# Kernel optimization log

Hardware: AMD Instinct MI355X
Metric: run time of the kernel (lower is better)

Reference implementation:

```python
import jax, jax.numpy as jnp
import numpy as np

N, HID, K = 256, 64, 2
B, T_ENC, T_DEC = 64, 12, 12
IN_DIM, OUT_DIM = 2, 1
NUM_SUPPORTS = 2
M = NUM_SUPPORTS * K + 1  # identity + K hops per support


def setup_inputs() -> dict:
    key = jax.random.key(0)
    ks = jax.random.split(key, 16)

    def w(k, shape, scale=0.05):
        return jax.random.normal(k, shape, dtype=jnp.float32) * scale

    def support(k):
        S = jax.random.uniform(k, (N, N), dtype=jnp.float32)
        return S / jnp.sum(S, axis=1, keepdims=True)  # random-walk normalized

    F0e = IN_DIM + HID   # encoder layer-0 concat(input, hidden) feature dim
    F1 = HID + HID       # layer-1 feature dim
    F0d = OUT_DIM + HID  # decoder layer-0 feature dim
    return {
        "encoder_inputs": jax.random.normal(ks[0], (B, T_ENC, N, IN_DIM), dtype=jnp.float32),
        "decoder_inputs": jax.random.normal(ks[1], (B, T_DEC, N, OUT_DIM), dtype=jnp.float32),
        "support0": support(ks[2]),
        "support1": support(ks[3]),
        "enc0_Wg": w(ks[4], (F0e, M, 2 * HID)), "enc0_bg": jnp.ones((2 * HID,), jnp.float32),
        "enc0_Wc": w(ks[5], (F0e, M, HID)),     "enc0_bc": jnp.zeros((HID,), jnp.float32),
        "enc1_Wg": w(ks[6], (F1, M, 2 * HID)),  "enc1_bg": jnp.ones((2 * HID,), jnp.float32),
        "enc1_Wc": w(ks[7], (F1, M, HID)),      "enc1_bc": jnp.zeros((HID,), jnp.float32),
        "dec0_Wg": w(ks[8], (F0d, M, 2 * HID)), "dec0_bg": jnp.ones((2 * HID,), jnp.float32),
        "dec0_Wc": w(ks[9], (F0d, M, HID)),     "dec0_bc": jnp.zeros((HID,), jnp.float32),
        "dec1_Wg": w(ks[10], (F1, M, 2 * HID)), "dec1_bg": jnp.ones((2 * HID,), jnp.float32),
        "dec1_Wc": w(ks[11], (F1, M, HID)),     "dec1_bc": jnp.zeros((HID,), jnp.float32),
        "proj_W": w(ks[12], (HID, OUT_DIM), 0.1),
        "proj_b": jnp.zeros((OUT_DIM,), jnp.float32),
    }


def _diff_conv(supports, x, h, W, b, in_dim):
    # x: (B, N*in_dim), h: (B, N*HID), W: (F, M, O) matching torch flatten order (f*M+m)
    Bsz = x.shape[0]
    xs = jnp.concatenate([x.reshape(Bsz, N, in_dim), h.reshape(Bsz, N, HID)], axis=-1)
    mats = [xs]
    for S in supports:
        x0 = xs
        x1 = jnp.einsum('mn,bnf->bmf', S, xs)
        mats.append(x1)
        for _ in range(2, K + 1):
            x2 = 2.0 * jnp.einsum('mn,bnf->bmf', S, x1) - x0  # Chebyshev recurrence
            mats.append(x2)
            x1, x0 = x2, x1
    X = jnp.stack(mats, axis=2)  # (B, N, M, F)
    out = jnp.einsum('bnmf,fmo->bno', X, W) + b
    return out.reshape(Bsz, -1)


def _cell(supports, x, h, Wg, bg, Wc, bc, in_dim):
    # DCGRUCell: sigmoid gates from diffusion conv, tanh candidate, GRU update
    Bsz = x.shape[0]
    ru = jax.nn.sigmoid(_diff_conv(supports, x, h, Wg, bg, in_dim)).reshape(Bsz, N, 2 * HID)
    r = ru[..., :HID].reshape(Bsz, N * HID)
    u = ru[..., HID:].reshape(Bsz, N * HID)
    c = jnp.tanh(_diff_conv(supports, x, r * h, Wc, bc, in_dim))
    return u * h + (1.0 - u) * c


def _forward(encoder_inputs, decoder_inputs, support0, support1,
             enc0_Wg, enc0_bg, enc0_Wc, enc0_bc, enc1_Wg, enc1_bg, enc1_Wc, enc1_bc,
             dec0_Wg, dec0_bg, dec0_Wc, dec0_bc, dec1_Wg, dec1_bg, dec1_Wc, dec1_bc,
             proj_W, proj_b):
    sup = (support0, support1)
    Bsz = encoder_inputs.shape[0]
    # encoder: (B,T,N,D) -> (T,B,N*D); zero initial hidden
    cur = jnp.transpose(encoder_inputs, (1, 0, 2, 3)).reshape(T_ENC, Bsz, N * IN_DIM)
    enc_params = [(enc0_Wg, enc0_bg, enc0_Wc, enc0_bc, IN_DIM),
                  (enc1_Wg, enc1_bg, enc1_Wc, enc1_bc, HID)]
    h_enc = []
    for (Wg, bg, Wc, bc, ind) in enc_params:
        h0 = jnp.zeros((Bsz, N * HID), cur.dtype)
        def estep(h, x, Wg=Wg, bg=bg, Wc=Wc, bc=bc, ind=ind):
            hn = _cell(sup, x, h, Wg, bg, Wc, bc, ind)
            return hn, hn
        hT, cur = jax.lax.scan(estep, h0, cur)
        h_enc.append(hT)
    # decoder (eval mode: no teacher forcing, dropout off); go symbol = zeros
    dec_params = [(dec0_Wg, dec0_bg, dec0_Wc, dec0_bc, OUT_DIM),
                  (dec1_Wg, dec1_bg, dec1_Wc, dec1_bc, HID)]
    go = jnp.zeros((Bsz, N * OUT_DIM), cur.dtype)

    def dstep(carry, _):
        hs, cur_in = carry
        out = cur_in
        new_hs = []
        for i, (Wg, bg, Wc, bc, ind) in enumerate(dec_params):
            hn = _cell(sup, out, hs[i], Wg, bg, Wc, bc, ind)
            out = hn
            new_hs.append(hn)
        proj = (jnp.einsum('bnh,ho->bno', out.reshape(Bsz, N, HID), proj_W) + proj_b)
        proj = proj.reshape(Bsz, N * OUT_DIM)
        return ((new_hs[0], new_hs[1]), proj), proj

    _, outs = jax.lax.scan(dstep, ((h_enc[0], h_enc[1]), go), None, length=T_DEC)
    outs = outs.reshape(T_DEC, Bsz, N, OUT_DIM)
    return jnp.transpose(outs, (1, 0, 2, 3))  # (B, T_DEC, N, OUT_DIM)


def reference(encoder_inputs, decoder_inputs, support0, support1,
              enc0_Wg, enc0_bg, enc0_Wc, enc0_bc, enc1_Wg, enc1_bg, enc1_Wc, enc1_bc,
              dec0_Wg, dec0_bg, dec0_Wc, dec0_bc, dec1_Wg, dec1_bg, dec1_Wc, dec1_bc,
              proj_W, proj_b):
    return _forward(encoder_inputs, decoder_inputs, support0, support1,
                    enc0_Wg, enc0_bg, enc0_Wc, enc0_bc, enc1_Wg, enc1_bg, enc1_Wc, enc1_bc,
                    dec0_Wg, dec0_bg, dec0_Wc, dec0_bc, dec1_Wg, dec1_bg, dec1_Wc, dec1_bc,
                    proj_W, proj_b)
```

## Files before the change

kernel.cpp:

```cpp
#include <hip/hip_runtime.h>
#include <stdint.h>


typedef short short8 __attribute__((ext_vector_type(8)));
typedef float f32x4 __attribute__((ext_vector_type(4)));
typedef unsigned short ushort4v __attribute__((ext_vector_type(4)));
typedef unsigned long long u64;
typedef u64 u64x2 __attribute__((ext_vector_type(2)));

#define DEVI __device__ __forceinline__

DEVI unsigned short f2bf(float x) {
  unsigned int u = __builtin_bit_cast(unsigned int, x);
  u += 0x7FFFu + ((u >> 16) & 1u);
  return (unsigned short)(u >> 16);
}
DEVI u64 ald(const u64* p) { return __hip_atomic_load(p, __ATOMIC_RELAXED, __HIP_MEMORY_SCOPE_AGENT); }
DEVI void ast(u64* p, u64 v) { __hip_atomic_store(p, v, __ATOMIC_RELAXED, __HIP_MEMORY_SCOPE_AGENT); }
DEVI float aldf(const float* p) { return __hip_atomic_load(p, __ATOMIC_RELAXED, __HIP_MEMORY_SCOPE_AGENT); }
DEVI void astf(float* p, float v) { __hip_atomic_store(p, v, __ATOMIC_RELAXED, __HIP_MEMORY_SCOPE_AGENT); }

struct KP {
  const float* enc_in;
  const float* sup0; const float* sup1;
  const float* Wsrc[8];
  const float* bias[8];
  const float* prW; const float* prB;
  float* out;
  unsigned short* A;
  unsigned short* Wp[8];
  unsigned short* H0[2];
  unsigned short* H1[2];
  unsigned short* RH0;
  unsigned short* RH1;
  float* XD;
  unsigned* ctr;
};

__global__ void prep(KP p) {
  const int i = blockIdx.x, tid = threadIdx.x;
  {
    const int s = i & 1, r = i >> 1;
    const float* S = s ? p.sup1 : p.sup0;
    float acc = 0.f;
    for (int k = 0; k < 256; ++k) acc = fmaf(S[r * 256 + k], S[k * 256 + tid], acc);
    p.A[(2 * s + 0) * 65536 + r * 256 + tid] = f2bf(S[r * 256 + tid]);
    p.A[(2 * s + 1) * 65536 + r * 256 + tid] = f2bf(2.f * acc - (r == tid ? 1.f : 0.f));
  }
  {
    const int gtid = i * 256 + tid;
    const int Fs[8]  = {66, 66, 128, 128, 65, 65, 128, 128};
    const int Os[8]  = {128, 64, 128, 64, 128, 64, 128, 64};
    const int FPs[8] = {96, 96, 128, 128, 96, 96, 128, 128};
    for (int w = 0; w < 8; ++w) {
      const int FPw = FPs[w], KPw = 5 * FPw, tot = Os[w] * KPw;
      for (int e = gtid; e < tot; e += 512 * 256) {
        const int o = e / KPw, k2 = e - o * KPw, m = k2 / FPw, f = k2 - m * FPw;
        p.Wp[w][e] = f2bf((f < Fs[w]) ? p.Wsrc[w][(f * 5 + m) * Os[w] + o] : 0.f);
      }
    }
  }
  {
    const int gtid = i * 256 + tid;
    u64* z0 = (u64*)p.H0[0];
    u64* z1 = (u64*)p.H1[0];
    ast(z0 + 2 * gtid, 0); ast(z0 + 2 * gtid + 1, 0);
    ast(z1 + 2 * gtid, 0); ast(z1 + 2 * gtid + 1, 0);
  }
  if (i == 0 && tid < 64)
    __hip_atomic_store(p.ctr + tid * 64, 0u, __ATOMIC_RELAXED, __HIP_MEMORY_SCOPE_AGENT);
}

template<int IND, int FP, int MODE>
DEVI void dc_stage(int b, int n0, int tid,
                   const float* xf32,
                   const unsigned short* xbf,
                   const unsigned short* hrows,
                   const unsigned short* Amats,
                   const unsigned short* Wp, const float* bias,
                   f32x4 (&hreg)[2], f32x4 (&ureg)[2],
                   unsigned short* grows,
                   const float* projW, const float* projB,
                   float* outp, float* xdout,
                   unsigned short* xsT, unsigned short* Hbuf)
{
  constexpr int F = IND + 64;
  constexpr int O = (MODE == 0) ? 128 : 64;
  constexpr int KPW = 5 * FP;
  constexpr int XS = 264;
  constexpr int HS = 136;
  constexpr int NFT = FP / 16;
  constexpr int NOT_ = O / 16;
  constexpr int FT_W = (NFT + 3) / 4;
  constexpr int OT_W = (NOT_ + 3) / 4;

  const int wv8 = tid >> 6, ln = tid & 63;
  const int l15 = ln & 15, l4 = ln >> 4;
  const int wr = wv8 & 1, wc = wv8 >> 1;
  const int r0 = wr * 32;

  {
    u64 la[4], lb[4];
    const u64* src = (const u64*)hrows;
#pragma unroll
    for (int it = 0; it < 4; ++it) { const int g = tid + it * 512; la[it] = ald(src + 2 * g); lb[it] = ald(src + 2 * g + 1); }
#pragma unroll
    for (int it = 0; it < 4; ++it) {
      const int g = tid + it * 512, row = g >> 5, c = g & 31;
      u64x2 v; v[0] = la[it]; v[1] = lb[it];
      *reinterpret_cast<u64x2*>(&xsT[(IND + row) * XS + c * 8]) = v;
    }
  }
  if (IND == 64) {
    u64 la[4], lb[4];
    const u64* src = (const u64*)xbf;
#pragma unroll
    for (int it = 0; it < 4; ++it) { const int g = tid + it * 512; la[it] = ald(src + 2 * g); lb[it] = ald(src + 2 * g + 1); }
#pragma unroll
    for (int it = 0; it < 4; ++it) {
      const int g = tid + it * 512, row = g >> 5, c = g & 31;
      u64x2 v; v[0] = la[it]; v[1] = lb[it];
      *reinterpret_cast<u64x2*>(&xsT[row * XS + c * 8]) = v;
    }
  } else if (IND == 2) {
    const float v = xf32[tid];
    xsT[(tid & 1) * XS + (tid >> 1)] = f2bf(v);
  } else {
    if (tid < 256) xsT[tid] = xf32 ? f2bf(aldf(xf32 + tid)) : (unsigned short)0;
  }
  if (F < FP) {
    for (int e = tid; e < (FP - F) * 256; e += 512)
      xsT[(F + (e >> 8)) * XS + (e & 255)] = 0;
  }
  __syncthreads();
#pragma unroll
  for (int it = 0; it < FP / 8; ++it) {
    const int e = tid + it * 512, f = e >> 6, nl = e & 63;
    Hbuf[nl * HS + f] = xsT[f * XS + n0 + nl];
  }
  __syncthreads();

  f32x4 pacc[2][OT_W];
#pragma unroll
  for (int rt = 0; rt < 2; ++rt)
#pragma unroll
    for (int oi = 0; oi < OT_W; ++oi) pacc[rt][oi] = 0.f;

  auto proj_step = [&](int m) {
#pragma unroll
    for (int k0 = 0; k0 < FP; k0 += 32) {
      short8 af[2];
#pragma unroll
      for (int rt = 0; rt < 2; ++rt)
        af[rt] = *reinterpret_cast<const short8*>(&Hbuf[(r0 + rt * 16 + l15) * HS + k0 + l4 * 8]);
#pragma unroll
      for (int oi = 0; oi < OT_W; ++oi) {
        const int ot = wc + 4 * oi;
        if (ot < NOT_) {
          short8 bf = *reinterpret_cast<const short8*>(&Wp[(ot * 16 + l15) * KPW + m * FP + k0 + l4 * 8]);
#pragma unroll
          for (int rt = 0; rt < 2; ++rt)
            pacc[rt][oi] = __builtin_amdgcn_mfma_f32_16x16x32_bf16(af[rt], bf, pacc[rt][oi], 0, 0, 0);
        }
      }
    }
  };

  proj_step(0);

  for (int mi = 0; mi < 4; ++mi) {
    const unsigned short* Am = Amats + mi * 65536;
    f32x4 hacc[2][FT_W];
#pragma unroll
    for (int rt = 0; rt < 2; ++rt)
#pragma unroll
      for (int fi = 0; fi < FT_W; ++fi) hacc[rt][fi] = 0.f;

#pragma unroll
    for (int k0 = 0; k0 < 256; k0 += 32) {
      short8 af[2];
#pragma unroll
      for (int rt = 0; rt < 2; ++rt)
        af[rt] = *reinterpret_cast<const short8*>(&Am[(n0 + r0 + rt * 16 + l15) * 256 + k0 + l4 * 8]);
#pragma unroll
      for (int fi = 0; fi < FT_W; ++fi) {
        const int ft = wc + 4 * fi;
        if (ft < NFT) {
          short8 bf = *reinterpret_cast<const short8*>(&xsT[(ft * 16 + l15) * XS + k0 + l4 * 8]);
#pragma unroll
          for (int rt = 0; rt < 2; ++rt)
            hacc[rt][fi] = __builtin_amdgcn_mfma_f32_16x16x32_bf16(af[rt], bf, hacc[rt][fi], 0, 0, 0);
        }
      }
    }
    __syncthreads();
#pragma unroll
    for (int fi = 0; fi < FT_W; ++fi) {
      const int ft = wc + 4 * fi;
      if (ft < NFT) {
#pragma unroll
        for (int rt = 0; rt < 2; ++rt)
#pragma unroll
          for (int j = 0; j < 4; ++j)
            Hbuf[(r0 + rt * 16 + l4 * 4 + j) * HS + ft * 16 + l15] = f2bf(hacc[rt][fi][j]);
      }
    }
    __syncthreads();
    proj_step(mi + 1);
  }

  if (MODE == 0) {
    const float br = bias[wc * 16 + l15];
    const float bu = bias[64 + wc * 16 + l15];
#pragma unroll
    for (int rt = 0; rt < 2; ++rt) {
      f32x4 uu;
      ushort4v pk;
#pragma unroll
      for (int jj = 0; jj < 4; ++jj) {
        const float r = 1.f / (1.f + __expf(-(pacc[rt][0][jj] + br)));
        uu[jj] = 1.f / (1.f + __expf(-(pacc[rt][1][jj] + bu)));
        pk[jj] = f2bf(r * hreg[rt][jj]);
      }
      ureg[rt] = uu;
      ast((u64*)(grows + (wc * 16 + l15) * 256 + n0 + r0 + rt * 16 + l4 * 4),
          __builtin_bit_cast(u64, pk));
    }
  } else {
    float* hrow = reinterpret_cast<float*>(Hbuf);
    if (MODE == 2) __syncthreads();
    const float bc = bias[wc * 16 + l15];
#pragma unroll
    for (int rt = 0; rt < 2; ++rt) {
      f32x4 hn;
      ushort4v pk;
#pragma unroll
      for (int jj = 0; jj < 4; ++jj) {
        const float ex = __expf(2.f * (pacc[rt][0][jj] + bc));
        const float c = 1.f - 2.f / (ex + 1.f);
        hn[jj] = ureg[rt][jj] * hreg[rt][jj] + (1.f - ureg[rt][jj]) * c;
        pk[jj] = f2bf(hn[jj]);
      }
      hreg[rt] = hn;
      ast((u64*)(grows + (wc * 16 + l15) * 256 + n0 + r0 + rt * 16 + l4 * 4),
          __builtin_bit_cast(u64, pk));
      if (MODE == 2) {
#pragma unroll
        for (int jj = 0; jj < 4; ++jj)
          hrow[(r0 + rt * 16 + l4 * 4 + jj) * 68 + wc * 16 + l15] = hn[jj];
      }
    }
    if (MODE == 2) {
      __syncthreads();
      if (tid < 64) {
        float acc = projB[0];
        const float* hr = hrow + tid * 68;
#pragma unroll
        for (int hid = 0; hid < 64; ++hid) acc = fmaf(hr[hid], projW[hid], acc);
        outp[b * 3072 + n0 + tid] = acc;
        astf(xdout + b * 256 + n0 + tid, acc);
      }
    }
  }
}

__launch_bounds__(512, 2)
__global__ void dcrnn_main(KP p) {
  __shared__ __align__(16) unsigned short xsT[128 * 264];
  __shared__ __align__(16) unsigned short Hbuf[64 * 136];
  const int tid = threadIdx.x;
  const int i = (int)blockIdx.x;
  const int q = (i >> 3) & 3;
  const int b = (i & 7) + 8 * (i >> 5);
  const int n0 = q * 64;

  unsigned* ctr = p.ctr + b * 64;
  unsigned st = 0;
  auto BAR = [&]() {
    ++st;
    asm volatile("s_waitcnt vmcnt(0)" ::: "memory");
    __syncthreads();
    if (tid == 0) {
      __hip_atomic_fetch_add(ctr, 1u, __ATOMIC_RELAXED, __HIP_MEMORY_SCOPE_AGENT);
      const unsigned target = st * 4u;
      while (__hip_atomic_load(ctr, __ATOMIC_RELAXED, __HIP_MEMORY_SCOPE_AGENT) < target)
        __builtin_amdgcn_s_sleep(2);
    }
    __syncthreads();
  };

  f32x4 h0[2], h1[2], u[2];
#pragma unroll
  for (int rt = 0; rt < 2; ++rt) { h0[rt] = 0.f; h1[rt] = 0.f; u[rt] = 0.f; }
  int c0 = 0, c1 = 0;

  for (int t = 0; t < 12; ++t) {
    const float* x0 = p.enc_in + (b * 12 + t) * 512;
    dc_stage<2, 96, 0>(b, n0, tid, x0, nullptr, p.H0[c0] + b * 16384, p.A, p.Wp[0], p.bias[0],
                       h0, u, p.RH0 + b * 16384, nullptr, nullptr, nullptr, nullptr, xsT, Hbuf);
    BAR();
    dc_stage<2, 96, 1>(b, n0, tid, x0, nullptr, p.RH0 + b * 16384, p.A, p.Wp[1], p.bias[1],
                       h0, u, p.H0[c0 ^ 1] + b * 16384, nullptr, nullptr, nullptr, nullptr, xsT, Hbuf);
    BAR(); c0 ^= 1;
    dc_stage<64, 128, 0>(b, n0, tid, nullptr, p.H0[c0] + b * 16384, p.H1[c1] + b * 16384, p.A, p.Wp[2], p.bias[2],
                         h1, u, p.RH1 + b * 16384, nullptr, nullptr, nullptr, nullptr, xsT, Hbuf);
    BAR();
    dc_stage<64, 128, 1>(b, n0, tid, nullptr, p.H0[c0] + b * 16384, p.RH1 + b * 16384, p.A, p.Wp[3], p.bias[3],
                         h1, u, p.H1[c1 ^ 1] + b * 16384, nullptr, nullptr, nullptr, nullptr, xsT, Hbuf);
    BAR(); c1 ^= 1;
  }

  for (int t = 0; t < 12; ++t) {
    const float* xd = t ? (p.XD + b * 256) : nullptr;
    dc_stage<1, 96, 0>(b, n0, tid, xd, nullptr, p.H0[c0] + b * 16384, p.A, p.Wp[4], p.bias[4],
                       h0, u, p.RH0 + b * 16384, nullptr, nullptr, nullptr, nullptr, xsT, Hbuf);
    BAR();
    dc_stage<1, 96, 1>(b, n0, tid, xd, nullptr, p.RH0 + b * 16384, p.A, p.Wp[5], p.bias[5],
                       h0, u, p.H0[c0 ^ 1] + b * 16384, nullptr, nullptr, nullptr, nullptr, xsT, Hbuf);
    BAR(); c0 ^= 1;
    dc_stage<64, 128, 0>(b, n0, tid, nullptr, p.H0[c0] + b * 16384, p.H1[c1] + b * 16384, p.A, p.Wp[6], p.bias[6],
                         h1, u, p.RH1 + b * 16384, nullptr, nullptr, nullptr, nullptr, xsT, Hbuf);
    BAR();
    dc_stage<64, 128, 2>(b, n0, tid, nullptr, p.H0[c0] + b * 16384, p.RH1 + b * 16384, p.A, p.Wp[7], p.bias[7],
                         h1, u, p.H1[c1 ^ 1] + b * 16384, p.prW, p.prB, p.out + t * 256, p.XD, xsT, Hbuf);
    if (t != 11) BAR();
    c1 ^= 1;
  }
}

extern "C" void kernel_launch(void* const* d_in, const int* in_sizes, int n_in,
                              void* d_out, int out_size, void* d_ws, size_t ws_size,
                              hipStream_t stream)
{
  (void)in_sizes; (void)n_in; (void)out_size; (void)ws_size;
  KP p;
  p.enc_in = (const float*)d_in[0];
  p.sup0 = (const float*)d_in[2];
  p.sup1 = (const float*)d_in[3];
  p.Wsrc[0] = (const float*)d_in[4];  p.bias[0] = (const float*)d_in[5];
  p.Wsrc[1] = (const float*)d_in[6];  p.bias[1] = (const float*)d_in[7];
  p.Wsrc[2] = (const float*)d_in[8];  p.bias[2] = (const float*)d_in[9];
  p.Wsrc[3] = (const float*)d_in[10]; p.bias[3] = (const float*)d_in[11];
  p.Wsrc[4] = (const float*)d_in[12]; p.bias[4] = (const float*)d_in[13];
  p.Wsrc[5] = (const float*)d_in[14]; p.bias[5] = (const float*)d_in[15];
  p.Wsrc[6] = (const float*)d_in[16]; p.bias[6] = (const float*)d_in[17];
  p.Wsrc[7] = (const float*)d_in[18]; p.bias[7] = (const float*)d_in[19];
  p.prW = (const float*)d_in[20];
  p.prB = (const float*)d_in[21];
  p.out = (float*)d_out;

  char* ws = (char*)d_ws;
  size_t off = 0;
  auto carve = [&](size_t bytes) -> char* {
    char* qp = ws + off;
    off += (bytes + 255) & ~(size_t)255;
    return qp;
  };
  p.A = (unsigned short*)carve(4 * 65536 * 2);
  p.Wp[0] = (unsigned short*)carve(128 * 480 * 2);
  p.Wp[1] = (unsigned short*)carve(64 * 480 * 2);
  p.Wp[2] = (unsigned short*)carve(128 * 640 * 2);
  p.Wp[3] = (unsigned short*)carve(64 * 640 * 2);
  p.Wp[4] = (unsigned short*)carve(128 * 480 * 2);
  p.Wp[5] = (unsigned short*)carve(64 * 480 * 2);
  p.Wp[6] = (unsigned short*)carve(128 * 640 * 2);
  p.Wp[7] = (unsigned short*)carve(64 * 640 * 2);
  p.H0[0] = (unsigned short*)carve(64 * 64 * 256 * 2);
  p.H0[1] = (unsigned short*)carve(64 * 64 * 256 * 2);
  p.H1[0] = (unsigned short*)carve(64 * 64 * 256 * 2);
  p.H1[1] = (unsigned short*)carve(64 * 64 * 256 * 2);
  p.RH0 = (unsigned short*)carve(64 * 64 * 256 * 2);
  p.RH1 = (unsigned short*)carve(64 * 64 * 256 * 2);
  p.XD = (float*)carve(64 * 256 * 4);
  p.ctr = (unsigned*)carve(64 * 256);

  prep<<<dim3(512), dim3(256), 0, stream>>>(p);
  dcrnn_main<<<dim3(256), dim3(512), 0, stream>>>(p);
}
```

Before: 2.305 ms.

## Split each batch across eight blocks and interleave two batches per block

Each block now owns 32 nodes of two batch elements instead of 64 nodes of one. It alternates the stages of the two batches, so the cross-block barrier for one batch is waited on while the other batch's stage runs, which hides the spin-wait latency. The Hbuf scratch is double-buffered to drop a syncthreads per hop, and launch bounds drop to one block per CU. The risk is more blocks per batch, higher barrier arrival counts, and half-size MFMA tiles that reuse less of each A fragment load.

```diff
diff --git a/kernel.cpp b/kernel.cpp
--- a/kernel.cpp
+++ b/kernel.cpp
@@ -78,7 +78,7 @@
                    const unsigned short* hrows,
                    const unsigned short* Amats,
                    const unsigned short* Wp, const float* bias,
-                   f32x4 (&hreg)[2], f32x4 (&ureg)[2],
+                   f32x4& hreg, f32x4& ureg,
                    unsigned short* grows,
                    const float* projW, const float* projB,
                    float* outp, float* xdout,
@@ -89,6 +89,7 @@
   constexpr int KPW = 5 * FP;
   constexpr int XS = 264;
   constexpr int HS = 136;
+  constexpr int HB = 32 * HS;
   constexpr int NFT = FP / 16;
   constexpr int NOT_ = O / 16;
   constexpr int FT_W = (NFT + 3) / 4;
@@ -97,7 +98,7 @@
   const int wv8 = tid >> 6, ln = tid & 63;
   const int l15 = ln & 15, l4 = ln >> 4;
   const int wr = wv8 & 1, wc = wv8 >> 1;
-  const int r0 = wr * 32;
+  const int r0 = wr * 16;
 
   {
     u64 la[4], lb[4];
@@ -133,126 +134,101 @@
       xsT[(F + (e >> 8)) * XS + (e & 255)] = 0;
   }
   __syncthreads();
-#pragma unroll
-  for (int it = 0; it < FP / 8; ++it) {
-    const int e = tid + it * 512, f = e >> 6, nl = e & 63;
+  for (int e = tid; e < FP * 32; e += 512) {
+    const int f = e >> 5, nl = e & 31;
     Hbuf[nl * HS + f] = xsT[f * XS + n0 + nl];
   }
   __syncthreads();
 
-  f32x4 pacc[2][OT_W];
-#pragma unroll
-  for (int rt = 0; rt < 2; ++rt)
-#pragma unroll
-    for (int oi = 0; oi < OT_W; ++oi) pacc[rt][oi] = 0.f;
-
-  auto proj_step = [&](int m) {
+  f32x4 pacc[OT_W];
+#pragma unroll
+  for (int oi = 0; oi < OT_W; ++oi) pacc[oi] = 0.f;
+
+  auto proj_step = [&](int m, const unsigned short* hb) {
 #pragma unroll
     for (int k0 = 0; k0 < FP; k0 += 32) {
-      short8 af[2];
-#pragma unroll
-      for (int rt = 0; rt < 2; ++rt)
-        af[rt] = *reinterpret_cast<const short8*>(&Hbuf[(r0 + rt * 16 + l15) * HS + k0 + l4 * 8]);
+      short8 af = *reinterpret_cast<const short8*>(&hb[(r0 + l15) * HS + k0 + l4 * 8]);
 #pragma unroll
       for (int oi = 0; oi < OT_W; ++oi) {
         const int ot = wc + 4 * oi;
         if (ot < NOT_) {
           short8 bf = *reinterpret_cast<const short8*>(&Wp[(ot * 16 + l15) * KPW + m * FP + k0 + l4 * 8]);
-#pragma unroll
-          for (int rt = 0; rt < 2; ++rt)
-            pacc[rt][oi] = __builtin_amdgcn_mfma_f32_16x16x32_bf16(af[rt], bf, pacc[rt][oi], 0, 0, 0);
+          pacc[oi] = __builtin_amdgcn_mfma_f32_16x16x32_bf16(af, bf, pacc[oi], 0, 0, 0);
         }
       }
     }
   };
 
-  proj_step(0);
+  proj_step(0, Hbuf);
 
   for (int mi = 0; mi < 4; ++mi) {
     const unsigned short* Am = Amats + mi * 65536;
-    f32x4 hacc[2][FT_W];
-#pragma unroll
-    for (int rt = 0; rt < 2; ++rt)
-#pragma unroll
-      for (int fi = 0; fi < FT_W; ++fi) hacc[rt][fi] = 0.f;
+    f32x4 hacc[FT_W];
+#pragma unroll
+    for (int fi = 0; fi < FT_W; ++fi) hacc[fi] = 0.f;
 
 #pragma unroll
     for (int k0 = 0; k0 < 256; k0 += 32) {
-      short8 af[2];
-#pragma unroll
-      for (int rt = 0; rt < 2; ++rt)
-        af[rt] = *reinterpret_cast<const short8*>(&Am[(n0 + r0 + rt * 16 + l15) * 256 + k0 + l4 * 8]);
+      short8 af = *reinterpret_cast<const short8*>(&Am[(n0 + r0 + l15) * 256 + k0 + l4 * 8]);
 #pragma unroll
       for (int fi = 0; fi < FT_W; ++fi) {
         const int ft = wc + 4 * fi;
         if (ft < NFT) {
           short8 bf = *reinterpret_cast<const short8*>(&xsT[(ft * 16 + l15) * XS + k0 + l4 * 8]);
-#pragma unroll
-          for (int rt = 0; rt < 2; ++rt)
-            hacc[rt][fi] = __builtin_amdgcn_mfma_f32_16x16x32_bf16(af[rt], bf, hacc[rt][fi], 0, 0, 0);
+          hacc[fi] = __builtin_amdgcn_mfma_f32_16x16x32_bf16(af, bf, hacc[fi], 0, 0, 0);
         }
       }
     }
-    __syncthreads();
+    unsigned short* dst = Hbuf + ((mi + 1) & 1) * HB;
 #pragma unroll
     for (int fi = 0; fi < FT_W; ++fi) {
       const int ft = wc + 4 * fi;
       if (ft < NFT) {
 #pragma unroll
-        for (int rt = 0; rt < 2; ++rt)
-#pragma unroll
-          for (int j = 0; j < 4; ++j)
-            Hbuf[(r0 + rt * 16 + l4 * 4 + j) * HS + ft * 16 + l15] = f2bf(hacc[rt][fi][j]);
+        for (int j = 0; j < 4; ++j)
+          dst[(r0 + l4 * 4 + j) * HS + ft * 16 + l15] = f2bf(hacc[fi][j]);
       }
     }
     __syncthreads();
-    proj_step(mi + 1);
+    proj_step(mi + 1, dst);
   }
 
   if (MODE == 0) {
     const float br = bias[wc * 16 + l15];
     const float bu = bias[64 + wc * 16 + l15];
-#pragma unroll
-    for (int rt = 0; rt < 2; ++rt) {
-      f32x4 uu;
-      ushort4v pk;
-#pragma unroll
-      for (int jj = 0; jj < 4; ++jj) {
-        const float r = 1.f / (1.f + __expf(-(pacc[rt][0][jj] + br)));
-        uu[jj] = 1.f / (1.f + __expf(-(pacc[rt][1][jj] + bu)));
-        pk[jj] = f2bf(r * hreg[rt][jj]);
-      }
-      ureg[rt] = uu;
-      ast((u64*)(grows + (wc * 16 + l15) * 256 + n0 + r0 + rt * 16 + l4 * 4),
-          __builtin_bit_cast(u64, pk));
-    }
+    f32x4 uu;
+    ushort4v pk;
+#pragma unroll
+    for (int jj = 0; jj < 4; ++jj) {
+      const float r = 1.f / (1.f + __expf(-(pacc[0][jj] + br)));
+      uu[jj] = 1.f / (1.f + __expf(-(pacc[1][jj] + bu)));
+      pk[jj] = f2bf(r * hreg[jj]);
+    }
+    ureg = uu;
+    ast((u64*)(grows + (wc * 16 + l15) * 256 + n0 + r0 + l4 * 4),
+        __builtin_bit_cast(u64, pk));
   } else {
     float* hrow = reinterpret_cast<float*>(Hbuf);
     if (MODE == 2) __syncthreads();
     const float bc = bias[wc * 16 + l15];
-#pragma unroll
-    for (int rt = 0; rt < 2; ++rt) {
-      f32x4 hn;
-      ushort4v pk;
-#pragma unroll
-      for (int jj = 0; jj < 4; ++jj) {
-        const float ex = __expf(2.f * (pacc[rt][0][jj] + bc));
-        const float c = 1.f - 2.f / (ex + 1.f);
-        hn[jj] = ureg[rt][jj] * hreg[rt][jj] + (1.f - ureg[rt][jj]) * c;
-        pk[jj] = f2bf(hn[jj]);
-      }
-      hreg[rt] = hn;
-      ast((u64*)(grows + (wc * 16 + l15) * 256 + n0 + r0 + rt * 16 + l4 * 4),
-          __builtin_bit_cast(u64, pk));
-      if (MODE == 2) {
-#pragma unroll
-        for (int jj = 0; jj < 4; ++jj)
-          hrow[(r0 + rt * 16 + l4 * 4 + jj) * 68 + wc * 16 + l15] = hn[jj];
-      }
-    }
+    f32x4 hn;
+    ushort4v pk;
+#pragma unroll
+    for (int jj = 0; jj < 4; ++jj) {
+      const float ex = __expf(2.f * (pacc[0][jj] + bc));
+      const float c = 1.f - 2.f / (ex + 1.f);
+      hn[jj] = ureg[jj] * hreg[jj] + (1.f - ureg[jj]) * c;
+      pk[jj] = f2bf(hn[jj]);
+    }
+    hreg = hn;
+    ast((u64*)(grows + (wc * 16 + l15) * 256 + n0 + r0 + l4 * 4),
+        __builtin_bit_cast(u64, pk));
     if (MODE == 2) {
+#pragma unroll
+      for (int jj = 0; jj < 4; ++jj)
+        hrow[(r0 + l4 * 4 + jj) * 68 + wc * 16 + l15] = hn[jj];
       __syncthreads();
-      if (tid < 64) {
+      if (tid < 32) {
         float acc = projB[0];
         const float* hr = hrow + tid * 68;
 #pragma unroll
@@ -264,68 +240,102 @@
   }
 }
 
-__launch_bounds__(512, 2)
+__launch_bounds__(512, 1)
 __global__ void dcrnn_main(KP p) {
   __shared__ __align__(16) unsigned short xsT[128 * 264];
-  __shared__ __align__(16) unsigned short Hbuf[64 * 136];
+  __shared__ __align__(16) unsigned short Hbuf[2 * 32 * 136];
   const int tid = threadIdx.x;
   const int i = (int)blockIdx.x;
-  const int q = (i >> 3) & 3;
-  const int b = (i & 7) + 8 * (i >> 5);
-  const int n0 = q * 64;
-
-  unsigned* ctr = p.ctr + b * 64;
+  const int xcd = i & 7, slot = i >> 3;
+  const int pr = xcd * 4 + (slot >> 3);
+  const int q = slot & 7;
+  const int b0 = 2 * pr, b1 = b0 + 1;
+  const int n0 = q * 32;
+
+  unsigned* ctr0 = p.ctr + b0 * 64;
+  unsigned* ctr1 = p.ctr + b1 * 64;
   unsigned st = 0;
-  auto BAR = [&]() {
-    ++st;
+
+  auto ARRIVEB = [&](unsigned* c) {
     asm volatile("s_waitcnt vmcnt(0)" ::: "memory");
     __syncthreads();
+    if (tid == 0) __hip_atomic_fetch_add(c, 1u, __ATOMIC_RELAXED, __HIP_MEMORY_SCOPE_AGENT);
+  };
+  auto WAITB = [&](unsigned* c, unsigned target) {
     if (tid == 0) {
-      __hip_atomic_fetch_add(ctr, 1u, __ATOMIC_RELAXED, __HIP_MEMORY_SCOPE_AGENT);
-      const unsigned target = st * 4u;
-      while (__hip_atomic_load(ctr, __ATOMIC_RELAXED, __HIP_MEMORY_SCOPE_AGENT) < target)
-        __builtin_amdgcn_s_sleep(2);
+      while (__hip_atomic_load(c, __ATOMIC_RELAXED, __HIP_MEMORY_SCOPE_AGENT) < target)
+        __builtin_amdgcn_s_sleep(1);
     }
     __syncthreads();
   };
 
-  f32x4 h0[2], h1[2], u[2];
-#pragma unroll
-  for (int rt = 0; rt < 2; ++rt) { h0[rt] = 0.f; h1[rt] = 0.f; u[rt] = 0.f; }
+#define DO_PAIR(CALL0, CALL1)                          \
+  {                                                    \
+    if (st) WAITB(ctr0, st * 8u);                      \
+    CALL0; ARRIVEB(ctr0);                              \
+    if (st) WAITB(ctr1, st * 8u);                      \
+    CALL1; ARRIVEB(ctr1);                              \
+    ++st;                                              \
+  }
+
+  f32x4 h0a, h1a, ua, h0b, h1b, ub;
+  h0a = 0.f; h1a = 0.f; ua = 0.f; h0b = 0.f; h1b = 0.f; ub = 0.f;
   int c0 = 0, c1 = 0;
 
   for (int t = 0; t < 12; ++t) {
-    const float* x0 = p.enc_in + (b * 12 + t) * 512;
-    dc_stage<2, 96, 0>(b, n0, tid, x0, nullptr, p.H0[c0] + b * 16384, p.A, p.Wp[0], p.bias[0],
-                       h0, u, p.RH0 + b * 16384, nullptr, nullptr, nullptr, nullptr, xsT, Hbuf);
-    BAR();
-    dc_stage<2, 96, 1>(b, n0, tid, x0, nullptr, p.RH0 + b * 16384, p.A, p.Wp[1], p.bias[1],
-                       h0, u, p.H0[c0 ^ 1] + b * 16384, nullptr, nullptr, nullptr, nullptr, xsT, Hbuf);
-    BAR(); c0 ^= 1;
-    dc_stage<64, 128, 0>(b, n0, tid, nullptr, p.H0[c0] + b * 16384, p.H1[c1] + b * 16384, p.A, p.Wp[2], p.bias[2],
-                         h1, u, p.RH1 + b * 16384, nullptr, nullptr, nullptr, nullptr, xsT, Hbuf);
-    BAR();
-    dc_stage<64, 128, 1>(b, n0, tid, nullptr, p.H0[c0] + b * 16384, p.RH1 + b * 16384, p.A, p.Wp[3], p.bias[3],
-                         h1, u, p.H1[c1 ^ 1] + b * 16384, nullptr, nullptr, nullptr, nullptr, xsT, Hbuf);
-    BAR(); c1 ^= 1;
+    const float* xa = p.enc_in + (b0 * 12 + t) * 512;
+    const float* xb = p.enc_in + (b1 * 12 + t) * 512;
+    DO_PAIR(
+      (dc_stage<2, 96, 0>(b0, n0, tid, xa, nullptr, p.H0[c0] + b0 * 16384, p.A, p.Wp[0], p.bias[0],
+                          h0a, ua, p.RH0 + b0 * 16384, nullptr, nullptr, nullptr, nullptr, xsT, Hbuf)),
+      (dc_stage<2, 96, 0>(b1, n0, tid, xb, nullptr, p.H0[c0] + b1 * 16384, p.A, p.Wp[0], p.bias[0],
+                          h0b, ub, p.RH0 + b1 * 16384, nullptr, nullptr, nullptr, nullptr, xsT, Hbuf)));
+    DO_PAIR(
+      (dc_stage<2, 96, 1>(b0, n0, tid, xa, nullptr, p.RH0 + b0 * 16384, p.A, p.Wp[1], p.bias[1],
+                          h0a, ua, p.H0[c0 ^ 1] + b0 * 16384, nullptr, nullptr, nullptr, nullptr, xsT, Hbuf)),
+      (dc_stage<2, 96, 1>(b1, n0, tid, xb, nullptr, p.RH0 + b1 * 16384, p.A, p.Wp[1], p.bias[1],
+                          h0b, ub, p.H0[c0 ^ 1] + b1 * 16384, nullptr, nullptr, nullptr, nullptr, xsT, Hbuf)));
+    c0 ^= 1;
+    DO_PAIR(
+      (dc_stage<64, 128, 0>(b0, n0, tid, nullptr, p.H0[c0] + b0 * 16384, p.H1[c1] + b0 * 16384, p.A, p.Wp[2], p.bias[2],
+                            h1a, ua, p.RH1 + b0 * 16384, nullptr, nullptr, nullptr, nullptr, xsT, Hbuf)),
+      (dc_stage<64, 128, 0>(b1, n0, tid, nullptr, p.H0[c0] + b1 * 16384, p.H1[c1] + b1 * 16384, p.A, p.Wp[2], p.bias[2],
+                            h1b, ub, p.RH1 + b1 * 16384, nullptr, nullptr, nullptr, nullptr, xsT, Hbuf)));
+    DO_PAIR(
+      (dc_stage<64, 128, 1>(b0, n0, tid, nullptr, p.H0[c0] + b0 * 16384, p.RH1 + b0 * 16384, p.A, p.Wp[3], p.bias[3],
+                            h1a, ua, p.H1[c1 ^ 1] + b0 * 16384, nullptr, nullptr, nullptr, nullptr, xsT, Hbuf)),
+      (dc_stage<64, 128, 1>(b1, n0, tid, nullptr, p.H0[c0] + b1 * 16384, p.RH1 + b1 * 16384, p.A, p.Wp[3], p.bias[3],
+                            h1b, ub, p.H1[c1 ^ 1] + b1 * 16384, nullptr, nullptr, nullptr, nullptr, xsT, Hbuf)));
+    c1 ^= 1;
   }
 
   for (int t = 0; t < 12; ++t) {
-    const float* xd = t ? (p.XD + b * 256) : nullptr;
-    dc_stage<1, 96, 0>(b, n0, tid, xd, nullptr, p.H0[c0] + b * 16384, p.A, p.Wp[4], p.bias[4],
-                       h0, u, p.RH0 + b * 16384, nullptr, nullptr, nullptr, nullptr, xsT, Hbuf);
-    BAR();
-    dc_stage<1, 96, 1>(b, n0, tid, xd, nullptr, p.RH0 + b * 16384, p.A, p.Wp[5], p.bias[5],
-                       h0, u, p.H0[c0 ^ 1] + b * 16384, nullptr, nullptr, nullptr, nullptr, xsT, Hbuf);
-    BAR(); c0 ^= 1;
-    dc_stage<64, 128, 0>(b, n0, tid, nullptr, p.H0[c0] + b * 16384, p.H1[c1] + b * 16384, p.A, p.Wp[6], p.bias[6],
-                         h1, u, p.RH1 + b * 16384, nullptr, nullptr, nullptr, nullptr, xsT, Hbuf);
-    BAR();
-    dc_stage<64, 128, 2>(b, n0, tid, nullptr, p.H0[c0] + b * 16384, p.RH1 + b * 16384, p.A, p.Wp[7], p.bias[7],
-                         h1, u, p.H1[c1 ^ 1] + b * 16384, p.prW, p.prB, p.out + t * 256, p.XD, xsT, Hbuf);
-    if (t != 11) BAR();
+    const float* xda = t ? (p.XD + b0 * 256) : nullptr;
+    const float* xdb = t ? (p.XD + b1 * 256) : nullptr;
+    DO_PAIR(
+      (dc_stage<1, 96, 0>(b0, n0, tid, xda, nullptr, p.H0[c0] + b0 * 16384, p.A, p.Wp[4], p.bias[4],
+                          h0a, ua, p.RH0 + b0 * 16384, nullptr, nullptr, nullptr, nullptr, xsT, Hbuf)),
+      (dc_stage<1, 96, 0>(b1, n0, tid, xdb, nullptr, p.H0[c0] + b1 * 16384, p.A, p.Wp[4], p.bias[4],
+                          h0b, ub, p.RH0 + b1 * 16384, nullptr, nullptr, nullptr, nullptr, xsT, Hbuf)));
+    DO_PAIR(
+      (dc_stage<1, 96, 1>(b0, n0, tid, xda, nullptr, p.RH0 + b0 * 16384, p.A, p.Wp[5], p.bias[5],
+                          h0a, ua, p.H0[c0 ^ 1] + b0 * 16384, nullptr, nullptr, nullptr, nullptr, xsT, Hbuf)),
+      (dc_stage<1, 96, 1>(b1, n0, tid, xdb, nullptr, p.RH0 + b1 * 16384, p.A, p.Wp[5], p.bias[5],
+                          h0b, ub, p.H0[c0 ^ 1] + b1 * 16384, nullptr, nullptr, nullptr, nullptr, xsT, Hbuf)));
+    c0 ^= 1;
+    DO_PAIR(
+      (dc_stage<64, 128, 0>(b0, n0, tid, nullptr, p.H0[c0] + b0 * 16384, p.H1[c1] + b0 * 16384, p.A, p.Wp[6], p.bias[6],
+                            h1a, ua, p.RH1 + b0 * 16384, nullptr, nullptr, nullptr, nullptr, xsT, Hbuf)),
+      (dc_stage<64, 128, 0>(b1, n0, tid, nullptr, p.H0[c0] + b1 * 16384, p.H1[c1] + b1 * 16384, p.A, p.Wp[6], p.bias[6],
+                            h1b, ub, p.RH1 + b1 * 16384, nullptr, nullptr, nullptr, nullptr, xsT, Hbuf)));
+    DO_PAIR(
+      (dc_stage<64, 128, 2>(b0, n0, tid, nullptr, p.H0[c0] + b0 * 16384, p.RH1 + b0 * 16384, p.A, p.Wp[7], p.bias[7],
+                            h1a, ua, p.H1[c1 ^ 1] + b0 * 16384, p.prW, p.prB, p.out + t * 256, p.XD, xsT, Hbuf)),
+      (dc_stage<64, 128, 2>(b1, n0, tid, nullptr, p.H0[c0] + b1 * 16384, p.RH1 + b1 * 16384, p.A, p.Wp[7], p.bias[7],
+                            h1b, ub, p.H1[c1 ^ 1] + b1 * 16384, p.prW, p.prB, p.out + t * 256, p.XD, xsT, Hbuf)));
     c1 ^= 1;
   }
+#undef DO_PAIR
 }
 
 extern "C" void kernel_launch(void* const* d_in, const int* in_sizes, int n_in,
```

After: 3.268 ms. 41.8% more time.

## Double-buffer Hbuf to drop a barrier and batch coherent 16-byte loads

Applied to the files above, without the earlier changes.

Replaces the paired relaxed 64-bit atomic loads of hidden and input rows with single 128-bit global loads carrying sc0 sc1 cache bits, issuing both groups before one waitcnt. Hbuf is double-buffered so each diffusion hop's result is written to the alternate buffer, which removes one __syncthreads per hop. LDS use grows by another 64x136 bf16 buffer, which may affect the two-blocks-per-CU occupancy target. Correctness now relies on the sc bits giving the same cross-block visibility the atomics provided.

```diff
diff --git a/kernel.cpp b/kernel.cpp
--- a/kernel.cpp
+++ b/kernel.cpp
@@ -6,7 +6,7 @@
 typedef float f32x4 __attribute__((ext_vector_type(4)));
 typedef unsigned short ushort4v __attribute__((ext_vector_type(4)));
 typedef unsigned long long u64;
-typedef u64 u64x2 __attribute__((ext_vector_type(2)));
+typedef int i32x4 __attribute__((ext_vector_type(4)));
 
 #define DEVI __device__ __forceinline__
 
@@ -15,10 +15,15 @@
   u += 0x7FFFu + ((u >> 16) & 1u);
   return (unsigned short)(u >> 16);
 }
-DEVI u64 ald(const u64* p) { return __hip_atomic_load(p, __ATOMIC_RELAXED, __HIP_MEMORY_SCOPE_AGENT); }
 DEVI void ast(u64* p, u64 v) { __hip_atomic_store(p, v, __ATOMIC_RELAXED, __HIP_MEMORY_SCOPE_AGENT); }
 DEVI float aldf(const float* p) { return __hip_atomic_load(p, __ATOMIC_RELAXED, __HIP_MEMORY_SCOPE_AGENT); }
 DEVI void astf(float* p, float v) { __hip_atomic_store(p, v, __ATOMIC_RELAXED, __HIP_MEMORY_SCOPE_AGENT); }
+
+DEVI i32x4 ldg_sc01(const void* p) {
+  i32x4 r;
+  asm volatile("global_load_dwordx4 %0, %1, off sc0 sc1" : "=v"(r) : "v"(p));
+  return r;
+}
 
 struct KP {
   const float* enc_in;
@@ -89,6 +94,7 @@
   constexpr int KPW = 5 * FP;
   constexpr int XS = 264;
   constexpr int HS = 136;
+  constexpr int HB = 64 * HS;
   constexpr int NFT = FP / 16;
   constexpr int NOT_ = O / 16;
   constexpr int FT_W = (NFT + 3) / 4;
@@ -100,32 +106,34 @@
   const int r0 = wr * 32;
 
   {
-    u64 la[4], lb[4];
-    const u64* src = (const u64*)hrows;
-#pragma unroll
-    for (int it = 0; it < 4; ++it) { const int g = tid + it * 512; la[it] = ald(src + 2 * g); lb[it] = ald(src + 2 * g + 1); }
+    i32x4 va[4];
+#pragma unroll
+    for (int it = 0; it < 4; ++it)
+      va[it] = ldg_sc01(reinterpret_cast<const char*>(hrows) + (tid + it * 512) * 16);
+    i32x4 vb[4];
+    if (IND == 64) {
+#pragma unroll
+      for (int it = 0; it < 4; ++it)
+        vb[it] = ldg_sc01(reinterpret_cast<const char*>(xbf) + (tid + it * 512) * 16);
+    }
+    asm volatile("s_waitcnt vmcnt(0)" ::: "memory");
 #pragma unroll
     for (int it = 0; it < 4; ++it) {
       const int g = tid + it * 512, row = g >> 5, c = g & 31;
-      u64x2 v; v[0] = la[it]; v[1] = lb[it];
-      *reinterpret_cast<u64x2*>(&xsT[(IND + row) * XS + c * 8]) = v;
-    }
-  }
-  if (IND == 64) {
-    u64 la[4], lb[4];
-    const u64* src = (const u64*)xbf;
-#pragma unroll
-    for (int it = 0; it < 4; ++it) { const int g = tid + it * 512; la[it] = ald(src + 2 * g); lb[it] = ald(src + 2 * g + 1); }
-#pragma unroll
-    for (int it = 0; it < 4; ++it) {
-      const int g = tid + it * 512, row = g >> 5, c = g & 31;
-      u64x2 v; v[0] = la[it]; v[1] = lb[it];
-      *reinterpret_cast<u64x2*>(&xsT[row * XS + c * 8]) = v;
-    }
-  } else if (IND == 2) {
+      *reinterpret_cast<i32x4*>(&xsT[(IND + row) * XS + c * 8]) = va[it];
+    }
+    if (IND == 64) {
+#pragma unroll
+      for (int it = 0; it < 4; ++it) {
+        const int g = tid + it * 512, row = g >> 5, c = g & 31;
+        *reinterpret_cast<i32x4*>(&xsT[row * XS + c * 8]) = vb[it];
+      }
+    }
+  }
+  if (IND == 2) {
     const float v = xf32[tid];
     xsT[(tid & 1) * XS + (tid >> 1)] = f2bf(v);
-  } else {
+  } else if (IND == 1) {
     if (tid < 256) xsT[tid] = xf32 ? f2bf(aldf(xf32 + tid)) : (unsigned short)0;
   }
   if (F < FP) {
@@ -146,13 +154,13 @@
 #pragma unroll
     for (int oi = 0; oi < OT_W; ++oi) pacc[rt][oi] = 0.f;
 
-  auto proj_step = [&](int m) {
+  auto proj_step = [&](int m, const unsigned short* hb) {
 #pragma unroll
     for (int k0 = 0; k0 < FP; k0 += 32) {
       short8 af[2];
 #pragma unroll
       for (int rt = 0; rt < 2; ++rt)
-        af[rt] = *reinterpret_cast<const short8*>(&Hbuf[(r0 + rt * 16 + l15) * HS + k0 + l4 * 8]);
+        af[rt] = *reinterpret_cast<const short8*>(&hb[(r0 + rt * 16 + l15) * HS + k0 + l4 * 8]);
 #pragma unroll
       for (int oi = 0; oi < OT_W; ++oi) {
         const int ot = wc + 4 * oi;
@@ -166,7 +174,7 @@
     }
   };
 
-  proj_step(0);
+  proj_step(0, Hbuf);
 
   for (int mi = 0; mi < 4; ++mi) {
     const unsigned short* Am = Amats + mi * 65536;
@@ -193,7 +201,7 @@
         }
       }
     }
-    __syncthreads();
+    unsigned short* dst = Hbuf + ((mi + 1) & 1) * HB;
 #pragma unroll
     for (int fi = 0; fi < FT_W; ++fi) {
       const int ft = wc + 4 * fi;
@@ -202,11 +210,11 @@
         for (int rt = 0; rt < 2; ++rt)
 #pragma unroll
           for (int j = 0; j < 4; ++j)
-            Hbuf[(r0 + rt * 16 + l4 * 4 + j) * HS + ft * 16 + l15] = f2bf(hacc[rt][fi][j]);
+            dst[(r0 + rt * 16 + l4 * 4 + j) * HS + ft * 16 + l15] = f2bf(hacc[rt][fi][j]);
       }
     }
     __syncthreads();
-    proj_step(mi + 1);
+    proj_step(mi + 1, dst);
   }
 
   if (MODE == 0) {
@@ -267,7 +275,7 @@
 __launch_bounds__(512, 2)
 __global__ void dcrnn_main(KP p) {
   __shared__ __align__(16) unsigned short xsT[128 * 264];
-  __shared__ __align__(16) unsigned short Hbuf[64 * 136];
+  __shared__ __align__(16) unsigned short Hbuf[2 * 64 * 136];
   const int tid = threadIdx.x;
   const int i = (int)blockIdx.x;
   const int q = (i >> 3) & 3;
```

New measurement: 2.736 ms. 1.19x slower.
